# Optimization experiments

Measured on AMD Instinct MI355X. Metric: run time of the kernel, lower is better.

## Reference

```python
import jax, jax.numpy as jnp
import numpy as np

NEG = -1000000.0  # mask value used by the torch module


def setup_inputs() -> dict:
    key = jax.random.key(0)
    k1, k2, k3, k4 = jax.random.split(key, 4)
    B, Q, K, D = 16, 2048, 2048, 128
    queries = jax.random.normal(k1, (B, Q, D), dtype=jnp.float32)
    keys = jax.random.normal(k2, (B, K, D), dtype=jnp.float32)
    values = jax.random.normal(k3, (B, K, D), dtype=jnp.float32)
    valid_lens = jax.random.randint(k4, (B,), 0, K, dtype=jnp.int32)
    return {"queries": queries, "keys": keys, "values": values, "valid_lens": valid_lens}


def reference(queries, keys, values, valid_lens):
    d = queries.shape[-1]
    # scores: [B, Q, K]
    scores = jnp.einsum("bqd,bkd->bqk", queries, keys) / jnp.sqrt(jnp.float32(d))
    # mask key positions >= valid_len[b] with the same -1e6 value as torch
    kv_pos = jnp.arange(scores.shape[-1])  # [K]
    mask = kv_pos[None, None, :] < valid_lens[:, None, None]  # [B,1,K]
    scores = jnp.where(mask, scores, NEG)
    attn = jax.nn.softmax(scores, axis=-1)
    # dropout p=0.0 -> identity (module in eval)
    return jnp.einsum("bqk,bkd->bqd", attn, values)
```

## Files before the change

kernel.cpp:

```cpp
#include <hip/hip_runtime.h>
#include <hip/hip_bf16.h>

#define NB    16
#define NQ    2048
#define NKV   2048
#define DH    128
#define KVT   32
#define NT    64
#define TIMG  8192

typedef __attribute__((ext_vector_type(8)))  short  short8;
typedef __attribute__((ext_vector_type(4)))  float  f32x4;
typedef __attribute__((ext_vector_type(2)))  float  f32x2;
typedef __attribute__((ext_vector_type(16))) float  f32x16;
typedef __attribute__((ext_vector_type(2)))  unsigned int u32x2;

__device__ __forceinline__ unsigned short f2bf(float f) {
    union { float f; unsigned int u; } x; x.f = f;
    unsigned int r = (x.u + 0x7fffu + ((x.u >> 16) & 1u)) >> 16;
    return (unsigned short)r;
}

__device__ __forceinline__ float u2f(unsigned int u) {
    union { unsigned int u; float f; } x; x.u = u; return x.f;
}

__device__ __forceinline__ void load_lds16(const void* g, void* l) {
    __builtin_amdgcn_global_load_lds(
        (const __attribute__((address_space(1))) unsigned int*)g,
        (__attribute__((address_space(3))) unsigned int*)l, 16, 0, 0);
}

__global__ __launch_bounds__(256)
void preconv(const float* __restrict__ kg, const float* __restrict__ vg,
             const int* __restrict__ vlg, char* __restrict__ kws,
             char* __restrict__ vws) {
    const int tid = threadIdx.x;
    const int bid = blockIdx.x;
    const int b = bid & 15, t = bid >> 4;
    const int vl = vlg[b];
    const int nt = (vl == 0) ? NT : ((vl + KVT - 1) >> 5);
    if (t >= nt) return;

    const float* kb = kg + ((size_t)b * NKV + t * KVT) * DH;
    const float* vb = vg + ((size_t)b * NKV + t * KVT) * DH;
    char* kimg = kws + (size_t)(b * NT + t) * TIMG;
    char* vimg = vws + (size_t)(b * NT + t) * TIMG;

    #pragma unroll
    for (int p = 0; p < 2; ++p) {
        int idx = p * 256 + tid;
        int kv = idx >> 4, ch = idx & 15;
        f32x4 a = *(const f32x4*)(kb + kv * DH + ch * 8);
        f32x4 c = *(const f32x4*)(kb + kv * DH + ch * 8 + 4);
        union { short8 v; unsigned short u[8]; } w;
        #pragma unroll
        for (int j = 0; j < 4; ++j) { w.u[j] = f2bf(a[j]); w.u[4 + j] = f2bf(c[j]); }
        *(short8*)(kimg + kv * 256 + ((ch * 16) ^ ((kv & 15) << 4))) = w.v;
    }
    #pragma unroll
    for (int p = 0; p < 2; ++p) {
        int task = p * 256 + tid;
        int w = task & 3, d = task >> 2;
        union { short8 v; unsigned short u[8]; } o;
        #pragma unroll
        for (int j = 0; j < 8; ++j) o.u[j] = f2bf(vb[(w * 8 + j) * DH + d]);
        int byte = (d >> 2) * 256 + 16 * ((w + 4 * (d & 3)) ^ ((d >> 2) & 15));
        *(short8*)(vimg + byte) = o.v;
    }
}

__global__ __launch_bounds__(256, 3)
void attn32(const float* __restrict__ qg, const char* __restrict__ kws,
            const char* __restrict__ vws, const int* __restrict__ vlg,
            float* __restrict__ og, unsigned int* __restrict__ opart,
            float* __restrict__ ellg, int S) {
    __shared__ __align__(16) char smem[49152];

    const int tid  = threadIdx.x;
    const int lane = tid & 63;
    const int wv   = tid >> 6;
    const int l31  = lane & 31;
    const int h    = lane >> 5;

    const int bid = blockIdx.x;
    const int b  = bid & 15;
    const int qt = (bid >> 4) & 15;
    const int s  = bid >> 8;
    const int q0 = qt * 128 + wv * 32;
    const int vl = vlg[b];
    const int nt = (vl == 0) ? NT : ((vl + KVT - 1) >> 5);

    if (s >= nt) return;

    const float QS = 1.4426950408889634f * 0.08838834764831845f;
    short8 qw[8];
    {
        const float* qp = qg + ((size_t)b * NQ + q0 + l31) * DH + h * 8;
        #pragma unroll
        for (int c = 0; c < 8; ++c) {
            f32x4 a  = *(const f32x4*)(qp + c * 16);
            f32x4 bb = *(const f32x4*)(qp + c * 16 + 4);
            union { short8 v; unsigned short u[8]; } t;
            #pragma unroll
            for (int j = 0; j < 4; ++j) { t.u[j] = f2bf(a[j] * QS); t.u[4 + j] = f2bf(bb[j] * QS); }
            qw[c] = t.v;
        }
    }

    const float MASKV = (vl == 0) ? 0.0f : -1442695.0f;
    f32x16 oacc[4];
    #pragma unroll
    for (int d = 0; d < 4; ++d) oacc[d] = (f32x16)(0.0f);
    float esum = 0.f;

    const char* kbase = kws + (size_t)b * NT * TIMG;
    const char* vbase = vws + (size_t)b * NT * TIMG;

    auto issue = [&](int t, int slot) {
        const char* ks = kbase + (size_t)t * TIMG;
        const char* vs = vbase + (size_t)t * TIMG;
        char* kd = smem + slot * 8192;
        char* vd = smem + 24576 + slot * 8192;
        #pragma unroll
        for (int i = 0; i < 2; ++i) {
            int off = wv * 2048 + i * 1024;
            load_lds16(ks + off + lane * 16, kd + off);
        }
        #pragma unroll
        for (int i = 0; i < 2; ++i) {
            int off = wv * 2048 + i * 1024;
            load_lds16(vs + off + lane * 16, vd + off);
        }
    };

    issue(s, 0);
    if (s + S < nt) issue(s + S, 1);
    int slot = 0;
    const int l15s = (l31 & 15) << 4;

    for (int tt = s; tt < nt; tt += S) {
        if (tt + S < nt) asm volatile("s_waitcnt vmcnt(4)" ::: "memory");
        else             asm volatile("s_waitcnt vmcnt(0)" ::: "memory");
        __syncthreads();

        int t2 = tt + 2 * S;
        if (t2 < nt) issue(t2, slot == 0 ? 2 : slot - 1);

        const char* kb = smem + slot * 8192;
        const char* vb = smem + 24576 + slot * 8192;

        f32x16 sc = (f32x16)(0.0f);
        __builtin_amdgcn_s_setprio(1);
        #pragma unroll
        for (int c = 0; c < 8; ++c) {
            short8 kf = *(const short8*)(kb + l31 * 256 + ((c * 32 + h * 16) ^ l15s));
            sc = __builtin_amdgcn_mfma_f32_32x32x16_bf16(kf, qw[c], sc, 0, 0, 0);
        }
        __builtin_amdgcn_s_setprio(0);

        if (vl == 0 || tt == nt - 1) {
            int kvb = tt * 32 + 4 * h;
            #pragma unroll
            for (int r = 0; r < 16; ++r) {
                int kvg = kvb + (r & 3) + 8 * (r >> 2);
                if (kvg >= vl) sc[r] = MASKV;
            }
        }

        float pe[16];
        #pragma unroll
        for (int r = 0; r < 16; ++r) pe[r] = __builtin_amdgcn_exp2f(sc[r]);
        esum += (((pe[0] + pe[1]) + (pe[2] + pe[3])) + ((pe[4] + pe[5]) + (pe[6] + pe[7])))
              + (((pe[8] + pe[9]) + (pe[10] + pe[11])) + ((pe[12] + pe[13]) + (pe[14] + pe[15])));

        unsigned int A, B, C, D, E, F, G, H;
        asm("v_cvt_pk_bf16_f32 %0, %1, %2" : "=v"(A) : "v"(pe[0]),  "v"(pe[1]));
        asm("v_cvt_pk_bf16_f32 %0, %1, %2" : "=v"(B) : "v"(pe[2]),  "v"(pe[3]));
        asm("v_cvt_pk_bf16_f32 %0, %1, %2" : "=v"(C) : "v"(pe[4]),  "v"(pe[5]));
        asm("v_cvt_pk_bf16_f32 %0, %1, %2" : "=v"(D) : "v"(pe[6]),  "v"(pe[7]));
        asm("v_cvt_pk_bf16_f32 %0, %1, %2" : "=v"(E) : "v"(pe[8]),  "v"(pe[9]));
        asm("v_cvt_pk_bf16_f32 %0, %1, %2" : "=v"(F) : "v"(pe[10]), "v"(pe[11]));
        asm("v_cvt_pk_bf16_f32 %0, %1, %2" : "=v"(G) : "v"(pe[12]), "v"(pe[13]));
        asm("v_cvt_pk_bf16_f32 %0, %1, %2" : "=v"(H) : "v"(pe[14]), "v"(pe[15]));
        asm("v_permlane32_swap_b32 %0, %1" : "+v"(A), "+v"(C));
        asm("v_permlane32_swap_b32 %0, %1" : "+v"(B), "+v"(D));
        asm("v_permlane32_swap_b32 %0, %1" : "+v"(E), "+v"(G));
        asm("v_permlane32_swap_b32 %0, %1" : "+v"(F), "+v"(H));
        union { short8 v; unsigned int w[4]; } P0, P1;
        P0.w[0] = A; P0.w[1] = B; P0.w[2] = C; P0.w[3] = D;
        P1.w[0] = E; P1.w[1] = F; P1.w[2] = G; P1.w[3] = H;
        short8 pa[2] = { P0.v, P1.v };

        __builtin_amdgcn_s_setprio(1);
        #pragma unroll
        for (int dblk = 0; dblk < 4; ++dblk) {
            int quad = dblk * 8 + (l31 >> 2);
            int xk = quad & 15;
            #pragma unroll
            for (int c16 = 0; c16 < 2; ++c16) {
                int w = c16 * 2 + h;
                short8 vf = *(const short8*)(vb + quad * 256 +
                                             16 * ((w + 4 * (l31 & 3)) ^ xk));
                oacc[dblk] = __builtin_amdgcn_mfma_f32_32x32x16_bf16(vf, pa[c16], oacc[dblk], 0, 0, 0);
            }
        }
        __builtin_amdgcn_s_setprio(0);

        slot = (slot == 2) ? 0 : slot + 1;
    }

    float ea = esum, eb;
    asm volatile("v_mov_b32 %0, %1" : "=v"(eb) : "v"(esum));
    asm("v_permlane32_swap_b32 %0, %1" : "+v"(ea), "+v"(eb));
    float ell = ea + eb;

    __syncthreads();

    if (S > 1 && lane < 32)
        ellg[(size_t)s * NB * NQ + (size_t)b * NQ + q0 + lane] = ell;

    float* tw = (float*)smem + wv * 1120;
    if (lane < 32) tw[1088 + l31] = 1.0f / ell;
    unsigned int* opw = opart + ((size_t)s * NB * NQ + (size_t)b * NQ + q0) * 64;
    float* ogp = og + ((size_t)b * NQ + q0) * DH;

    #pragma unroll
    for (int dblk = 0; dblk < 4; ++dblk) {
        #pragma unroll
        for (int r = 0; r < 16; ++r) {
            int dd = (r & 3) + 8 * (r >> 2) + 4 * h;
            tw[l31 * 34 + dd] = oacc[dblk][r];
        }
        asm volatile("s_waitcnt lgkmcnt(0)" ::: "memory");
        #pragma unroll
        for (int pp = 0; pp < 8; ++pp) {
            int qq = pp * 4 + (lane >> 4);
            int cc = lane & 15;
            f32x2 v = *(f32x2*)(tw + qq * 34 + cc * 2);
            if (S == 1) {
                float rl = tw[1088 + qq];
                f32x2 o = { v[0] * rl, v[1] * rl };
                *(f32x2*)(ogp + (size_t)qq * DH + dblk * 32 + cc * 2) = o;
            } else {
                unsigned int w;
                asm("v_cvt_pk_bf16_f32 %0, %1, %2" : "=v"(w) : "v"(v[0]), "v"(v[1]));
                opw[(size_t)qq * 64 + dblk * 16 + cc] = w;
            }
        }
        asm volatile("s_waitcnt lgkmcnt(0)" ::: "memory");
    }
}

__global__ __launch_bounds__(256)
void combine(const unsigned int* __restrict__ opart, const float* __restrict__ ellg,
             const int* __restrict__ vlg, float* __restrict__ og, int S) {
    int idx = blockIdx.x * 256 + threadIdx.x;
    int row = idx >> 5;
    int c   = idx & 31;
    int b   = row >> 11;
    int vl  = vlg[b];
    int nact = (vl == 0) ? NT : ((vl + KVT - 1) >> 5);
    if (nact > S) nact = S;
    float a0 = 0.f, a1 = 0.f, a2 = 0.f, a3 = 0.f, l = 0.f;
    for (int s = 0; s < nact; ++s) {
        l += ellg[(size_t)s * NB * NQ + row];
        u32x2 w = *(const u32x2*)(opart + ((size_t)s * NB * NQ + row) * 64 + c * 2);
        a0 += u2f(w[0] << 16); a1 += u2f(w[0] & 0xffff0000u);
        a2 += u2f(w[1] << 16); a3 += u2f(w[1] & 0xffff0000u);
    }
    float rl = 1.0f / l;
    f32x4 o = { a0 * rl, a1 * rl, a2 * rl, a3 * rl };
    *(f32x4*)(og + (size_t)row * DH + c * 4) = o;
}

extern "C" void kernel_launch(void* const* d_in, const int* in_sizes, int n_in,
                              void* d_out, int out_size, void* d_ws, size_t ws_size,
                              hipStream_t stream) {
    const float* q  = (const float*)d_in[0];
    const float* k  = (const float*)d_in[1];
    const float* v  = (const float*)d_in[2];
    const int*   vl = (const int*)d_in[3];
    float* o = (float*)d_out;

    const size_t IMG     = (size_t)NB * NT * TIMG;
    const size_t ELL_OFF = 2 * IMG;
    const size_t ELL_MAX = (size_t)4 * NB * NQ * 4;
    const size_t OP_OFF  = ELL_OFF + ELL_MAX;
    const size_t OP_ONE  = (size_t)NB * NQ * DH * 2;

    int S = 1;
    if      (ws_size >= OP_OFF + 4 * OP_ONE) S = 4;
    else if (ws_size >= OP_OFF + 2 * OP_ONE) S = 2;

    char* kws = (char*)d_ws;
    char* vws = (char*)d_ws + IMG;
    float* ellg = (float*)((char*)d_ws + ELL_OFF);
    unsigned int* opart = (unsigned int*)((char*)d_ws + OP_OFF);

    preconv<<<dim3(NB * NT), dim3(256), 0, stream>>>(k, v, vl, kws, vws);
    attn32<<<dim3(256 * S), dim3(256), 0, stream>>>(q, kws, vws, vl, o, opart, ellg, S);
    if (S > 1)
        combine<<<dim3(NB * NQ * 32 / 256), dim3(256), 0, stream>>>(opart, ellg, vl, o, S);
}
```

Before: 60.88 us.

## Make each wave an independent work item with private double-buffered LDS

Each wave now owns a separate (batch, query chunk, split) item and its own 32KB LDS region. It loads the full K/V tiles itself into two private buffers and never calls block-wide __syncthreads. The QK MFMA chain is split into two independent accumulators to shorten the dependency chain, and the s_setprio hints are removed. This gets rid of block barriers and lets waves in a block run on different split indices or stop early on their own. In exchange each wave issues four times as many loads, K/V sharing across waves in a block is lost, and 128KB of LDS limits occupancy to one block per CU.

```diff
diff --git a/kernel.cpp b/kernel.cpp
--- a/kernel.cpp
+++ b/kernel.cpp
@@ -70,12 +70,12 @@
     }
 }
 
-__global__ __launch_bounds__(256, 3)
+__global__ __launch_bounds__(256, 1)
 void attn32(const float* __restrict__ qg, const char* __restrict__ kws,
             const char* __restrict__ vws, const int* __restrict__ vlg,
             float* __restrict__ og, unsigned int* __restrict__ opart,
-            float* __restrict__ ellg, int S) {
-    __shared__ __align__(16) char smem[49152];
+            float* __restrict__ ellg, int S, int log2S) {
+    __shared__ __align__(16) char smem[131072];
 
     const int tid  = threadIdx.x;
     const int lane = tid & 63;
@@ -83,15 +83,19 @@
     const int l31  = lane & 31;
     const int h    = lane >> 5;
 
-    const int bid = blockIdx.x;
-    const int b  = bid & 15;
-    const int qt = (bid >> 4) & 15;
-    const int s  = bid >> 8;
-    const int q0 = qt * 128 + wv * 32;
-    const int vl = vlg[b];
-    const int nt = (vl == 0) ? NT : ((vl + KVT - 1) >> 5);
+    const int item = blockIdx.x * 4 + wv;
+    const int s    = item & (S - 1);
+    const int rest = item >> log2S;
+    const int b    = rest & 15;
+    const int qc   = rest >> 4;
+    const int q0   = qc * 32;
+    const int vl   = vlg[b];
+    const int nt   = (vl == 0) ? NT : ((vl + KVT - 1) >> 5);
 
     if (s >= nt) return;
+
+    char* myk = smem + wv * 32768;
+    char* myv = smem + wv * 32768 + 16384;
 
     const float QS = 1.4426950408889634f * 0.08838834764831845f;
     short8 qw[8];
@@ -120,44 +124,35 @@
     auto issue = [&](int t, int slot) {
         const char* ks = kbase + (size_t)t * TIMG;
         const char* vs = vbase + (size_t)t * TIMG;
-        char* kd = smem + slot * 8192;
-        char* vd = smem + 24576 + slot * 8192;
-        #pragma unroll
-        for (int i = 0; i < 2; ++i) {
-            int off = wv * 2048 + i * 1024;
-            load_lds16(ks + off + lane * 16, kd + off);
-        }
-        #pragma unroll
-        for (int i = 0; i < 2; ++i) {
-            int off = wv * 2048 + i * 1024;
-            load_lds16(vs + off + lane * 16, vd + off);
-        }
+        #pragma unroll
+        for (int i = 0; i < 8; ++i)
+            load_lds16(ks + i * 1024 + lane * 16, myk + slot * 8192 + i * 1024);
+        #pragma unroll
+        for (int i = 0; i < 8; ++i)
+            load_lds16(vs + i * 1024 + lane * 16, myv + slot * 8192 + i * 1024);
     };
 
     issue(s, 0);
     if (s + S < nt) issue(s + S, 1);
-    int slot = 0;
+    int p = 0;
     const int l15s = (l31 & 15) << 4;
 
     for (int tt = s; tt < nt; tt += S) {
-        if (tt + S < nt) asm volatile("s_waitcnt vmcnt(4)" ::: "memory");
+        if (tt + S < nt) asm volatile("s_waitcnt vmcnt(16)" ::: "memory");
         else             asm volatile("s_waitcnt vmcnt(0)" ::: "memory");
-        __syncthreads();
-
-        int t2 = tt + 2 * S;
-        if (t2 < nt) issue(t2, slot == 0 ? 2 : slot - 1);
-
-        const char* kb = smem + slot * 8192;
-        const char* vb = smem + 24576 + slot * 8192;
-
-        f32x16 sc = (f32x16)(0.0f);
-        __builtin_amdgcn_s_setprio(1);
-        #pragma unroll
-        for (int c = 0; c < 8; ++c) {
-            short8 kf = *(const short8*)(kb + l31 * 256 + ((c * 32 + h * 16) ^ l15s));
-            sc = __builtin_amdgcn_mfma_f32_32x32x16_bf16(kf, qw[c], sc, 0, 0, 0);
-        }
-        __builtin_amdgcn_s_setprio(0);
+
+        const char* kb = myk + p * 8192;
+        const char* vb = myv + p * 8192;
+
+        f32x16 sc0 = (f32x16)(0.0f), sc1 = (f32x16)(0.0f);
+        #pragma unroll
+        for (int c = 0; c < 4; ++c) {
+            short8 kfa = *(const short8*)(kb + l31 * 256 + (((2 * c) * 32 + h * 16) ^ l15s));
+            short8 kfb = *(const short8*)(kb + l31 * 256 + (((2 * c + 1) * 32 + h * 16) ^ l15s));
+            sc0 = __builtin_amdgcn_mfma_f32_32x32x16_bf16(kfa, qw[2 * c], sc0, 0, 0, 0);
+            sc1 = __builtin_amdgcn_mfma_f32_32x32x16_bf16(kfb, qw[2 * c + 1], sc1, 0, 0, 0);
+        }
+        f32x16 sc = sc0 + sc1;
 
         if (vl == 0 || tt == nt - 1) {
             int kvb = tt * 32 + 4 * h;
@@ -192,7 +187,6 @@
         P1.w[0] = E; P1.w[1] = F; P1.w[2] = G; P1.w[3] = H;
         short8 pa[2] = { P0.v, P1.v };
 
-        __builtin_amdgcn_s_setprio(1);
         #pragma unroll
         for (int dblk = 0; dblk < 4; ++dblk) {
             int quad = dblk * 8 + (l31 >> 2);
@@ -205,9 +199,10 @@
                 oacc[dblk] = __builtin_amdgcn_mfma_f32_32x32x16_bf16(vf, pa[c16], oacc[dblk], 0, 0, 0);
             }
         }
-        __builtin_amdgcn_s_setprio(0);
-
-        slot = (slot == 2) ? 0 : slot + 1;
+
+        asm volatile("s_waitcnt lgkmcnt(0)" ::: "memory");
+        if (tt + 2 * S < nt) issue(tt + 2 * S, p);
+        p ^= 1;
     }
 
     float ea = esum, eb;
@@ -215,12 +210,10 @@
     asm("v_permlane32_swap_b32 %0, %1" : "+v"(ea), "+v"(eb));
     float ell = ea + eb;
 
-    __syncthreads();
-
     if (S > 1 && lane < 32)
         ellg[(size_t)s * NB * NQ + (size_t)b * NQ + q0 + lane] = ell;
 
-    float* tw = (float*)smem + wv * 1120;
+    float* tw = (float*)(smem + wv * 32768);
     if (lane < 32) tw[1088 + l31] = 1.0f / ell;
     unsigned int* opw = opart + ((size_t)s * NB * NQ + (size_t)b * NQ + q0) * 64;
     float* ogp = og + ((size_t)b * NQ + q0) * DH;
@@ -289,9 +282,9 @@
     const size_t OP_OFF  = ELL_OFF + ELL_MAX;
     const size_t OP_ONE  = (size_t)NB * NQ * DH * 2;
 
-    int S = 1;
-    if      (ws_size >= OP_OFF + 4 * OP_ONE) S = 4;
-    else if (ws_size >= OP_OFF + 2 * OP_ONE) S = 2;
+    int S = 1, log2S = 0;
+    if      (ws_size >= OP_OFF + 4 * OP_ONE) { S = 4; log2S = 2; }
+    else if (ws_size >= OP_OFF + 2 * OP_ONE) { S = 2; log2S = 1; }
 
     char* kws = (char*)d_ws;
     char* vws = (char*)d_ws + IMG;
@@ -299,7 +292,7 @@
     unsigned int* opart = (unsigned int*)((char*)d_ws + OP_OFF);
 
     preconv<<<dim3(NB * NT), dim3(256), 0, stream>>>(k, v, vl, kws, vws);
-    attn32<<<dim3(256 * S), dim3(256), 0, stream>>>(q, kws, vws, vl, o, opart, ellg, S);
+    attn32<<<dim3(256 * S), dim3(256), 0, stream>>>(q, kws, vws, vl, o, opart, ellg, S, log2S);
     if (S > 1)
         combine<<<dim3(NB * NQ * 32 / 256), dim3(256), 0, stream>>>(opart, ellg, vl, o, S);
 }
```

Result: slower. 107.3 us (+76.3%).
